# Kernel optimization log

Measured on AMD Instinct MI355X. Metric: run time of the kernel, lower is better.

## Reference

```python
import jax, jax.numpy as jnp
import numpy as np

B, L, HID = 128, 256, 768
HID2 = 2 * HID
CDIM, SDIM, NPROJ = 192, 128, 128
FDIM = CDIM + SDIM + 1
BIG = 1e9  # finite pad so sorted invalid tokens go last without inf/nan issues


def setup_inputs() -> dict:
    key = jax.random.key(0)
    ks = jax.random.split(key, 12)
    H = jax.random.normal(ks[0], (B, L, HID), dtype=jnp.float32)
    tt = jax.random.randint(ks[1], (B, L), 0, 2, dtype=jnp.int32)
    m = jnp.ones((B, L), dtype=jnp.int32)
    s = 1.0 / np.sqrt(HID2)
    Wc = jax.random.uniform(ks[2], (CDIM, HID2), minval=-s, maxval=s, dtype=jnp.float32)
    bc = jax.random.uniform(ks[3], (CDIM,), minval=-s, maxval=s, dtype=jnp.float32)
    Ws = jax.random.uniform(ks[4], (SDIM, HID2), minval=-s, maxval=s, dtype=jnp.float32)
    bs = jax.random.uniform(ks[5], (SDIM,), minval=-s, maxval=s, dtype=jnp.float32)
    gate = jnp.array([0.5], dtype=jnp.float32)
    ln_g = jnp.ones((FDIM,), dtype=jnp.float32)
    ln_b = jnp.zeros((FDIM,), dtype=jnp.float32)
    sc = 1.0 / np.sqrt(FDIM)
    Wcls = jax.random.uniform(ks[6], (2, FDIM), minval=-sc, maxval=sc, dtype=jnp.float32)
    bcls = jax.random.uniform(ks[7], (2,), minval=-sc, maxval=sc, dtype=jnp.float32)
    d = jax.random.normal(ks[8], (NPROJ, HID), dtype=jnp.float32)
    proj_dirs = d / jnp.linalg.norm(d, axis=1, keepdims=True)
    return {"H": H, "tt": tt, "m": m, "Wc": Wc, "bc": bc, "Ws": Ws, "bs": bs,
            "gate": gate, "ln_g": ln_g, "ln_b": ln_b, "Wcls": Wcls, "bcls": bcls,
            "proj_dirs": proj_dirs}


def _forward(H, tt, m, Wc, bc, Ws, bs, gate, ln_g, ln_b, Wcls, bcls, proj_dirs):
    mask0 = (tt == 0) & (m == 1)  # [B,L]
    mask1 = (tt == 1) & (m == 1)
    f0 = mask0.astype(H.dtype)
    f1 = mask1.astype(H.dtype)
    cls = H[:, 0]  # [B,HID]
    mean0 = jnp.einsum('blh,bl->bh', H, f0) / jnp.clip(f0.sum(1, keepdims=True), 1.0)
    mean1 = jnp.einsum('blh,bl->bh', H, f1) / jnp.clip(f1.sum(1, keepdims=True), 1.0)
    rep = jnp.concatenate([cls, mean0 - mean1], axis=1)  # [B,2*HID]
    C = rep @ Wc.T + bc
    S = rep @ Ws.T + bs
    g = jax.nn.sigmoid(gate)  # [1]
    fused = jnp.concatenate([C * (1.0 - g), S * g], axis=1)

    # max-sliced W1 between token-type-0 and token-type-1 token sets, batched.
    P = jnp.einsum('blh,ph->blp', H, proj_dirs)  # [B,L,NPROJ]
    x0 = jnp.sort(jnp.where(mask0[..., None], P, BIG), axis=1)  # valid tokens first
    x1 = jnp.sort(jnp.where(mask1[..., None], P, BIG), axis=1)
    n0 = mask0.sum(1)
    n1 = mask1.sum(1)
    mcnt = jnp.minimum(n0, n1)  # [B]
    rmask = (jnp.arange(L)[None, :] < mcnt[:, None])[..., None]  # [B,L,1]
    diff = jnp.where(rmask, x0, 0.0) - jnp.where(rmask, x1, 0.0)
    mean_abs = jnp.abs(diff).sum(1) / jnp.maximum(mcnt, 1)[:, None].astype(P.dtype)  # [B,NPROJ]
    d_ot = mean_abs.max(axis=1, keepdims=True)  # [B,1]

    feat = jnp.concatenate([fused, d_ot], axis=1)  # [B,FDIM]
    mu = feat.mean(-1, keepdims=True)
    var = feat.var(-1, keepdims=True)
    normed = (feat - mu) * jax.lax.rsqrt(var + 1e-5) * ln_g + ln_b
    return normed @ Wcls.T + bcls  # [B,2]


def reference(H, tt, m, Wc, bc, Ws, bs, gate, ln_g, ln_b, Wcls, bcls, proj_dirs):
    return _forward(H, tt, m, Wc, bc, Ws, bs, gate, ln_g, ln_b, Wcls, bcls, proj_dirs)
```

## Files before the change

kernel.cpp:

```cpp
#include <hip/hip_runtime.h>
#include <cmath>

#define B_   128
#define L_   256
#define HID_ 768
#define HID2_ 1536
#define CDIM_ 192
#define SDIM_ 128
#define NPROJ_ 128
#define FDIM_ 321
#define KSL_ 384
#define PTSTRIDE ((size_t)B_ * NPROJ_ * L_)

typedef __attribute__((ext_vector_type(8))) short bf16x8;
typedef __attribute__((ext_vector_type(4))) float f32x4;

__device__ inline unsigned short bf_hi_trunc(float x) {
    return (unsigned short)(__float_as_uint(x) >> 16);
}
__device__ inline float bf2f(unsigned short s) {
    return __uint_as_float(((unsigned int)s) << 16);
}
__device__ inline unsigned short f2bf_rne(float x) {
    unsigned int u = __float_as_uint(x);
    unsigned int r = (u + 0x7fff + ((u >> 16) & 1)) >> 16;
    return (unsigned short)r;
}

__global__ __launch_bounds__(192) void pre_kernel(
    const float* __restrict__ Pd, unsigned short* __restrict__ Pjh,
    unsigned short* __restrict__ Pjl)
{
    int i = blockIdx.x * 192 + threadIdx.x;
    float4 v = ((const float4*)Pd)[i];
    ushort4 h, l;
    h.x = bf_hi_trunc(v.x); l.x = f2bf_rne(v.x - bf2f(h.x));
    h.y = bf_hi_trunc(v.y); l.y = f2bf_rne(v.y - bf2f(h.y));
    h.z = bf_hi_trunc(v.z); l.z = f2bf_rne(v.z - bf2f(h.z));
    h.w = bf_hi_trunc(v.w); l.w = f2bf_rne(v.w - bf2f(h.w));
    ((ushort4*)Pjh)[i] = h;
    ((ushort4*)Pjl)[i] = l;
}

__device__ inline void stats_bfly(float4 x, float4 y, float fa, float fb,
                                  int kbase, int lane, float* __restrict__ sacc)
{
    float px = x.x * fa + y.x * fb;
    float py = x.y * fa + y.y * fb;
    float pz = x.z * fa + y.z * fb;
    float pw = x.w * fa + y.w * fb;
#pragma unroll
    for (int off = 8; off < 64; off <<= 1) {
        px += __shfl_xor(px, off, 64);
        py += __shfl_xor(py, off, 64);
        pz += __shfl_xor(pz, off, 64);
        pw += __shfl_xor(pw, off, 64);
    }
    if (lane < 8) {
        float* d = &sacc[kbase + lane * 4];
        atomicAdd(d + 0, px);
        atomicAdd(d + 1, py);
        atomicAdd(d + 2, pz);
        atomicAdd(d + 3, pw);
    }
}

#define LDSROW 72
__global__ __launch_bounds__(256, 4) void gemm_mfma(
    const float* __restrict__ H, const unsigned short* __restrict__ Pjh,
    const unsigned short* __restrict__ Pjl, const int* __restrict__ tt,
    const int* __restrict__ mm, float* __restrict__ Ptp,
    float* __restrict__ part)
{
    __shared__ unsigned short Hs[2][64 * LDSROW];
    __shared__ float sacc[KSL_];
    __shared__ float sw[64];

    int tid = threadIdx.x;
    int w = tid >> 6;
    int lane = tid & 63;
    int c = lane & 15;
    int q = lane >> 4;

    int ks     = blockIdx.x & 1;
    int lchunk = (blockIdx.x >> 1) & 3;
    int b      = blockIdx.x >> 3;
    int lbase  = lchunk * 64;

    const float* Hbase = H + ((size_t)(b * L_ + lbase)) * HID_ + ks * KSL_;
    int hrow0 = tid >> 3;
    int hc4   = tid & 7;

    const unsigned short* pjh0 = Pjh + (size_t)(w * 32 + c) * HID_ + ks * KSL_ + q * 8;
    const unsigned short* pjh1 = pjh0 + (size_t)16 * HID_;
    const unsigned short* pjl0 = Pjl + (size_t)(w * 32 + c) * HID_ + ks * KSL_ + q * 8;
    const unsigned short* pjl1 = pjl0 + (size_t)16 * HID_;

    f32x4 acc[2][4] = {};

    float4 hA0, hA1, hB0, hB1;
    uint4 fhA0, fhA1, flA0, flA1;
    uint4 fhB0, fhB1, flB0, flB1;
    uint4 chh0, chh1, cll0, cll1;

#define LOADS(S, T) do {                                                      \
    int k0_ = (T) * 32;                                                       \
    h##S##0 = *(const float4*)(Hbase + (size_t)hrow0 * HID_ + k0_ + hc4 * 4); \
    h##S##1 = *(const float4*)(Hbase + (size_t)(hrow0 + 32) * HID_ + k0_ + hc4 * 4); \
    fh##S##0 = *(const uint4*)(pjh0 + k0_);                                   \
    fh##S##1 = *(const uint4*)(pjh1 + k0_);                                   \
    fl##S##0 = *(const uint4*)(pjl0 + k0_);                                   \
    fl##S##1 = *(const uint4*)(pjl1 + k0_);                                   \
} while (0)

#define CONVST(S, BUF, T) do {                                                \
    float4 v0_ = h##S##0, v1_ = h##S##1;                                      \
    ushort4 h0_, l0_, h1_, l1_;                                               \
    h0_.x = bf_hi_trunc(v0_.x); l0_.x = f2bf_rne(v0_.x - bf2f(h0_.x));        \
    h0_.y = bf_hi_trunc(v0_.y); l0_.y = f2bf_rne(v0_.y - bf2f(h0_.y));        \
    h0_.z = bf_hi_trunc(v0_.z); l0_.z = f2bf_rne(v0_.z - bf2f(h0_.z));        \
    h0_.w = bf_hi_trunc(v0_.w); l0_.w = f2bf_rne(v0_.w - bf2f(h0_.w));        \
    h1_.x = bf_hi_trunc(v1_.x); l1_.x = f2bf_rne(v1_.x - bf2f(h1_.x));        \
    h1_.y = bf_hi_trunc(v1_.y); l1_.y = f2bf_rne(v1_.y - bf2f(h1_.y));        \
    h1_.z = bf_hi_trunc(v1_.z); l1_.z = f2bf_rne(v1_.z - bf2f(h1_.z));        \
    h1_.w = bf_hi_trunc(v1_.w); l1_.w = f2bf_rne(v1_.w - bf2f(h1_.w));        \
    *(ushort4*)&Hs[BUF][hrow0 * LDSROW + hc4 * 4]             = h0_;          \
    *(ushort4*)&Hs[BUF][hrow0 * LDSROW + 32 + hc4 * 4]        = l0_;          \
    *(ushort4*)&Hs[BUF][(hrow0 + 32) * LDSROW + hc4 * 4]      = h1_;          \
    *(ushort4*)&Hs[BUF][(hrow0 + 32) * LDSROW + 32 + hc4 * 4] = l1_;          \
    stats_bfly(v0_, v1_, fa, fb, (T) * 32, lane, sacc);                       \
} while (0)

#define COPYF(S) do {                                                         \
    chh0 = fh##S##0; chh1 = fh##S##1; cll0 = fl##S##0; cll1 = fl##S##1;       \
} while (0)

#define GEMMSTEP(BUF) do {                                                    \
    bf16x8 bh_[4], bl_[4];                                                    \
    _Pragma("unroll")                                                         \
    for (int lt = 0; lt < 4; ++lt) {                                          \
        int l_ = lt * 16 + c;                                                 \
        bh_[lt] = *(const bf16x8*)&Hs[BUF][l_ * LDSROW + q * 8];              \
        bl_[lt] = *(const bf16x8*)&Hs[BUF][l_ * LDSROW + 32 + q * 8];         \
    }                                                                         \
    bf16x8 ah0_ = *(bf16x8*)&chh0, ah1_ = *(bf16x8*)&chh1;                    \
    bf16x8 al0_ = *(bf16x8*)&cll0, al1_ = *(bf16x8*)&cll1;                    \
    _Pragma("unroll")                                                         \
    for (int lt = 0; lt < 4; ++lt) {                                          \
        acc[0][lt] = __builtin_amdgcn_mfma_f32_16x16x32_bf16(ah0_, bh_[lt], acc[0][lt], 0, 0, 0); \
        acc[0][lt] = __builtin_amdgcn_mfma_f32_16x16x32_bf16(ah0_, bl_[lt], acc[0][lt], 0, 0, 0); \
        acc[0][lt] = __builtin_amdgcn_mfma_f32_16x16x32_bf16(al0_, bh_[lt], acc[0][lt], 0, 0, 0); \
        acc[1][lt] = __builtin_amdgcn_mfma_f32_16x16x32_bf16(ah1_, bh_[lt], acc[1][lt], 0, 0, 0); \
        acc[1][lt] = __builtin_amdgcn_mfma_f32_16x16x32_bf16(ah1_, bl_[lt], acc[1][lt], 0, 0, 0); \
        acc[1][lt] = __builtin_amdgcn_mfma_f32_16x16x32_bf16(al1_, bh_[lt], acc[1][lt], 0, 0, 0); \
    }                                                                         \
} while (0)

    LOADS(A, 0);
    LOADS(B, 1);

    int t_ = tt[b * L_ + tid];
    int m_ = mm[b * L_ + tid];
    int n0 = __syncthreads_count(t_ == 0 && m_ == 1);
    int n1 = __syncthreads_count(t_ == 1 && m_ == 1);
    float r0 = 1.f / fmaxf((float)n0, 1.f);
    float r1 = 1.f / fmaxf((float)n1, 1.f);
    if (tid < 64) {
        int tl = tt[b * L_ + lbase + tid];
        int ml = mm[b * L_ + lbase + tid];
        sw[tid] = ((tl == 0 && ml == 1) ? r0 : 0.f)
                - ((tl == 1 && ml == 1) ? r1 : 0.f);
    }
    for (int i = tid; i < KSL_; i += 256) sacc[i] = 0.f;
    __syncthreads();
    float fa = sw[hrow0], fb = sw[hrow0 + 32];

    CONVST(A, 0, 0);
    COPYF(A);
    __syncthreads();

    for (int p = 0; p < 6; ++p) {
        int t0 = 2 * p;
        if (t0 + 2 < 12) LOADS(A, t0 + 2);
        GEMMSTEP(0);
        CONVST(B, 1, t0 + 1);
        COPYF(B);
        __syncthreads();

        int t1 = t0 + 1;
        if (t1 + 2 < 12) LOADS(B, t1 + 2);
        GEMMSTEP(1);
        if (t1 + 1 < 12) {
            CONVST(A, 0, t1 + 1);
            COPYF(A);
        }
        __syncthreads();
    }

    float* Pts = Ptp + (size_t)ks * PTSTRIDE;
#pragma unroll
    for (int pt = 0; pt < 2; ++pt)
#pragma unroll
    for (int lt = 0; lt < 4; ++lt)
#pragma unroll
    for (int r = 0; r < 4; ++r) {
        int p2 = w * 32 + pt * 16 + q * 4 + r;
        int l = lbase + lt * 16 + c;
        Pts[((size_t)(b * NPROJ_ + p2)) * L_ + l] = acc[pt][lt][r];
    }

    {
        float* pdst = part + (size_t)(b * 4 + lchunk) * HID_ + ks * KSL_;
        for (int i = tid; i < KSL_; i += 256)
            pdst[i] = sacc[i];
    }
#undef LOADS
#undef CONVST
#undef COPYF
#undef GEMMSTEP
}

__global__ __launch_bounds__(256) void headot_kernel(
    const float* __restrict__ H, const int* __restrict__ tt,
    const int* __restrict__ mm, const float* __restrict__ part,
    const float* __restrict__ Wc, const float* __restrict__ bc,
    const float* __restrict__ Ws, const float* __restrict__ bs,
    const float* __restrict__ gate, const float* __restrict__ Ptp,
    float* __restrict__ fused, float* __restrict__ dist)
{
    if (blockIdx.x < B_ * 8) {
        __shared__ float srep[HID2_];
        int b = blockIdx.x >> 3;
        int ochunk = (blockIdx.x & 7) * 40;
        int tid = threadIdx.x;

        const float* pp = part + (size_t)b * 4 * HID_;
        for (int h = tid; h < HID_; h += 256) {
            float a = pp[h] + pp[HID_ + h] + pp[2 * HID_ + h] + pp[3 * HID_ + h];
            srep[h]        = H[(size_t)b * L_ * HID_ + h];
            srep[HID_ + h] = a;
        }
        __syncthreads();

        int w = tid >> 6;
        int lane = tid & 63;
        float g = 1.0f / (1.0f + expf(-gate[0]));

#pragma unroll
        for (int r = 0; r < 10; ++r) {
            int o = ochunk + r * 4 + w;
            bool isC = (o < CDIM_);
            const float4* wr = (const float4*)(isC ? (Wc + (size_t)o * HID2_)
                                                   : (Ws + (size_t)(o - CDIM_) * HID2_));
            float acc = 0.f;
#pragma unroll
            for (int u = 0; u < 6; ++u) {
                int k4 = lane + u * 64;
                float4 a = *(const float4*)&srep[k4 * 4];
                float4 ww = wr[k4];
                acc += a.x * ww.x + a.y * ww.y + a.z * ww.z + a.w * ww.w;
            }
            for (int off = 32; off; off >>= 1) acc += __shfl_xor(acc, off, 64);
            if (lane == 0) {
                float bias = isC ? bc[o] : bs[o - CDIM_];
                float scale = isC ? (1.0f - g) : g;
                fused[(size_t)b * (CDIM_ + SDIM_) + o] = (acc + bias) * scale;
            }
        }
        return;
    }

    int bid = blockIdx.x - B_ * 8;
    int w = bid * 4 + (threadIdx.x >> 6);
    int lane = threadIdx.x & 63;
    int b = w >> 7;
    int p = w & (NPROJ_ - 1);

    float4 pv0 = *(const float4*)(Ptp + ((size_t)(b * NPROJ_ + p)) * L_ + lane * 4);
    float4 pv1 = *(const float4*)(Ptp + PTSTRIDE + ((size_t)(b * NPROJ_ + p)) * L_ + lane * 4);
    float4 pv = make_float4(pv0.x + pv1.x, pv0.y + pv1.y, pv0.z + pv1.z, pv0.w + pv1.w);
    int4 t4 = *(const int4*)(tt + (size_t)b * L_ + lane * 4);
    int4 m4 = *(const int4*)(mm + (size_t)b * L_ + lane * 4);

    float pvals[4] = {pv.x, pv.y, pv.z, pv.w};
    int tv[4] = {t4.x, t4.y, t4.z, t4.w};
    int mv[4] = {m4.x, m4.y, m4.z, m4.w};

    unsigned key[4];
#pragma unroll
    for (int r = 0; r < 4; ++r) {
        unsigned u = __float_as_uint(pvals[r]);
        unsigned s = (u & 0x80000000u) ? ~u : (u | 0x80000000u);
        unsigned label = (mv[r] == 1) ? (unsigned)tv[r] : 2u;
        key[r] = (s & ~3u) | label;
    }

    {
        unsigned mn0 = min(key[0], key[1]), mx0 = max(key[0], key[1]);
        key[0] = mn0; key[1] = mx0;
        unsigned mn1 = min(key[2], key[3]), mx1 = max(key[2], key[3]);
        key[2] = mx1; key[3] = mn1;
    }
#pragma unroll
    for (int k = 4; k <= 256; k <<= 1) {
        bool up = (lane & (k >> 2)) == 0;
#pragma unroll
        for (int j = k >> 1; j >= 4; j >>= 1) {
            int lj = j >> 2;
#pragma unroll
            for (int r = 0; r < 4; ++r) {
                unsigned o = (unsigned)__shfl_xor((int)key[r], lj, 64);
                bool lower = (lane & lj) == 0;
                unsigned mn = min(key[r], o), mx = max(key[r], o);
                key[r] = (lower == up) ? mn : mx;
            }
        }
        {
            unsigned mn0 = min(key[0], key[2]), mx0 = max(key[0], key[2]);
            key[0] = up ? mn0 : mx0; key[2] = up ? mx0 : mn0;
            unsigned mn1 = min(key[1], key[3]), mx1 = max(key[1], key[3]);
            key[1] = up ? mn1 : mx1; key[3] = up ? mx1 : mn1;
        }
        {
            unsigned mn0 = min(key[0], key[1]), mx0 = max(key[0], key[1]);
            key[0] = up ? mn0 : mx0; key[1] = up ? mx0 : mn0;
            unsigned mn1 = min(key[2], key[3]), mx1 = max(key[2], key[3]);
            key[2] = up ? mn1 : mx1; key[3] = up ? mx1 : mn1;
        }
    }

    int lab[4];
    float tval[4];
    unsigned sincl[4];
    unsigned run = 0;
#pragma unroll
    for (int r = 0; r < 4; ++r) {
        lab[r] = (int)(key[r] & 3u);
        unsigned s = key[r] & ~3u;
        unsigned u = (s & 0x80000000u) ? (s ^ 0x80000000u) : ~s;
        tval[r] = __uint_as_float(u);
        unsigned unit = ((lab[r] == 0) ? 0x10000u : 0u) | ((lab[r] == 1) ? 1u : 0u);
        run += unit;
        sincl[r] = run;
    }
    unsigned inc = run;
#pragma unroll
    for (int d = 1; d < 64; d <<= 1) {
        unsigned tt2 = (unsigned)__shfl_up((int)inc, d, 64);
        if (lane >= d) inc += tt2;
    }
    unsigned ex = inc - run;
    unsigned total = (unsigned)__shfl((int)inc, 63, 64);
    int n0 = (int)(total >> 16), n1 = (int)(total & 0xffffu);
    int m = (n0 < n1) ? n0 : n1;

    float ssum = 0.f;
#pragma unroll
    for (int r = 0; r < 4; ++r) {
        unsigned C = ex + sincl[r];
        int c0 = (int)(C >> 16), c1 = (int)(C & 0xffffu);
        int s0 = (lab[r] == 0), s1 = (lab[r] == 1);
        int wi = abs(min(c0, m) - min(c1, m));
        int wp = abs(min(c0 - s0, m) - min(c1 - s1, m));
        ssum += tval[r] * (float)(wp - wi);
    }
    for (int off = 32; off; off >>= 1) ssum += __shfl_xor(ssum, off, 64);
    if (lane == 0) dist[b * NPROJ_ + p] = ssum / (float)((m > 1) ? m : 1);
}

__global__ __launch_bounds__(64) void final_kernel(
    const float* __restrict__ fused, const float* __restrict__ dist,
    const float* __restrict__ ln_g, const float* __restrict__ ln_b,
    const float* __restrict__ Wcls, const float* __restrict__ bcls,
    float* __restrict__ out)
{
    int b = blockIdx.x;
    int lane = threadIdx.x;

    float mx = fmaxf(dist[b * NPROJ_ + lane], dist[b * NPROJ_ + 64 + lane]);
    for (int off = 32; off; off >>= 1) mx = fmaxf(mx, __shfl_xor(mx, off, 64));

    float fv[6];
    float sum = 0.f, sq = 0.f;
#pragma unroll
    for (int u = 0; u < 6; ++u) {
        int j = lane + u * 64;
        float x = 0.f;
        if (j < CDIM_ + SDIM_) x = fused[(size_t)b * (CDIM_ + SDIM_) + j];
        else if (j == CDIM_ + SDIM_) x = mx;
        fv[u] = x;
        if (j < FDIM_) { sum += x; sq += x * x; }
    }
    for (int off = 32; off; off >>= 1) {
        sum += __shfl_xor(sum, off, 64);
        sq  += __shfl_xor(sq,  off, 64);
    }
    float mu = sum / (float)FDIM_;
    float var = sq / (float)FDIM_ - mu * mu;
    float inv = rsqrtf(var + 1e-5f);

    float d0 = 0.f, d1 = 0.f;
#pragma unroll
    for (int u = 0; u < 6; ++u) {
        int j = lane + u * 64;
        if (j < FDIM_) {
            float nx = (fv[u] - mu) * inv * ln_g[j] + ln_b[j];
            d0 += nx * Wcls[j];
            d1 += nx * Wcls[FDIM_ + j];
        }
    }
    for (int off = 32; off; off >>= 1) {
        d0 += __shfl_xor(d0, off, 64);
        d1 += __shfl_xor(d1, off, 64);
    }
    if (lane == 0) {
        out[b * 2 + 0] = d0 + bcls[0];
        out[b * 2 + 1] = d1 + bcls[1];
    }
}

extern "C" void kernel_launch(void* const* d_in, const int* in_sizes, int n_in,
                              void* d_out, int out_size, void* d_ws, size_t ws_size,
                              hipStream_t stream)
{
    const float* H    = (const float*)d_in[0];
    const int*   tt   = (const int*)d_in[1];
    const int*   mm   = (const int*)d_in[2];
    const float* Wc   = (const float*)d_in[3];
    const float* bc   = (const float*)d_in[4];
    const float* Ws   = (const float*)d_in[5];
    const float* bs   = (const float*)d_in[6];
    const float* gate = (const float*)d_in[7];
    const float* ln_g = (const float*)d_in[8];
    const float* ln_b = (const float*)d_in[9];
    const float* Wcls = (const float*)d_in[10];
    const float* bcls = (const float*)d_in[11];
    const float* Pd   = (const float*)d_in[12];
    float* out = (float*)d_out;

    float* ws = (float*)d_ws;
    float* Ptp   = ws;
    float* part  = Ptp + 2 * PTSTRIDE;
    float* fused = part + (size_t)B_ * 4 * HID_;
    float* dist  = fused + (size_t)B_ * (CDIM_ + SDIM_);
    unsigned short* Pjh = (unsigned short*)(dist + (size_t)B_ * NPROJ_);
    unsigned short* Pjl = Pjh + (size_t)NPROJ_ * HID_;

    pre_kernel<<<128, 192, 0, stream>>>(Pd, Pjh, Pjl);
    gemm_mfma<<<B_ * 8, 256, 0, stream>>>(H, Pjh, Pjl, tt, mm, Ptp, part);
    headot_kernel<<<B_ * 8 + B_ * NPROJ_ / 4, 256, 0, stream>>>(
        H, tt, mm, part, Wc, bc, Ws, bs, gate, Ptp, fused, dist);
    final_kernel<<<B_, 64, 0, stream>>>(fused, dist, ln_g, ln_b, Wcls, bcls, out);
}
```

Baseline: 246.5 us.

## Widen GEMM K-step to 64 with single-stage prefetch and halved barriers

Restructures the split-bf16 MFMA projection GEMM to process 64-wide K tiles per iteration instead of 32, cutting the loop from 12 to 6 steps and halving the number of __syncthreads barriers. The two-deep register prefetch (A/B sets) is replaced by a one-tile-ahead prefetch of double-size tiles, and the LDS row stride grows to hold 64 hi plus 64 lo values. Occupancy hint drops from 4 to 3 blocks per CU to accommodate the larger register and LDS footprint, which may reduce latency hiding.

```diff
diff --git a/kernel.cpp b/kernel.cpp
--- a/kernel.cpp
+++ b/kernel.cpp
@@ -65,14 +65,14 @@
     }
 }
 
-#define LDSROW 72
-__global__ __launch_bounds__(256, 4) void gemm_mfma(
+#define LDSROW64 136
+__global__ __launch_bounds__(256, 3) void gemm_mfma(
     const float* __restrict__ H, const unsigned short* __restrict__ Pjh,
     const unsigned short* __restrict__ Pjl, const int* __restrict__ tt,
     const int* __restrict__ mm, float* __restrict__ Ptp,
     float* __restrict__ part)
 {
-    __shared__ unsigned short Hs[2][64 * LDSROW];
+    __shared__ unsigned short Hs[2][64 * LDSROW64];
     __shared__ float sacc[KSL_];
     __shared__ float sw[64];
 
@@ -97,67 +97,83 @@
     const unsigned short* pjl1 = pjl0 + (size_t)16 * HID_;
 
     f32x4 acc[2][4] = {};
-
-    float4 hA0, hA1, hB0, hB1;
-    uint4 fhA0, fhA1, flA0, flA1;
-    uint4 fhB0, fhB1, flB0, flB1;
-    uint4 chh0, chh1, cll0, cll1;
-
-#define LOADS(S, T) do {                                                      \
-    int k0_ = (T) * 32;                                                       \
-    h##S##0 = *(const float4*)(Hbase + (size_t)hrow0 * HID_ + k0_ + hc4 * 4); \
-    h##S##1 = *(const float4*)(Hbase + (size_t)(hrow0 + 32) * HID_ + k0_ + hc4 * 4); \
-    fh##S##0 = *(const uint4*)(pjh0 + k0_);                                   \
-    fh##S##1 = *(const uint4*)(pjh1 + k0_);                                   \
-    fl##S##0 = *(const uint4*)(pjl0 + k0_);                                   \
-    fl##S##1 = *(const uint4*)(pjl1 + k0_);                                   \
+    float4 h0a, h0b, h1a, h1b;
+    uint4 cah[2][2], cal[2][2];
+    uint4 nah[2][2], nal[2][2];
+
+#define LOADT(T) do {                                                         \
+    int k0_ = (T) * 64;                                                       \
+    h0a = *(const float4*)(Hbase + (size_t)hrow0 * HID_ + k0_ + hc4 * 4);     \
+    h0b = *(const float4*)(Hbase + (size_t)hrow0 * HID_ + k0_ + 32 + hc4 * 4);\
+    h1a = *(const float4*)(Hbase + (size_t)(hrow0 + 32) * HID_ + k0_ + hc4 * 4);      \
+    h1b = *(const float4*)(Hbase + (size_t)(hrow0 + 32) * HID_ + k0_ + 32 + hc4 * 4); \
+    nah[0][0] = *(const uint4*)(pjh0 + k0_);                                  \
+    nah[0][1] = *(const uint4*)(pjh0 + k0_ + 32);                             \
+    nah[1][0] = *(const uint4*)(pjh1 + k0_);                                  \
+    nah[1][1] = *(const uint4*)(pjh1 + k0_ + 32);                             \
+    nal[0][0] = *(const uint4*)(pjl0 + k0_);                                  \
+    nal[0][1] = *(const uint4*)(pjl0 + k0_ + 32);                             \
+    nal[1][0] = *(const uint4*)(pjl1 + k0_);                                  \
+    nal[1][1] = *(const uint4*)(pjl1 + k0_ + 32);                             \
 } while (0)
 
-#define CONVST(S, BUF, T) do {                                                \
-    float4 v0_ = h##S##0, v1_ = h##S##1;                                      \
-    ushort4 h0_, l0_, h1_, l1_;                                               \
-    h0_.x = bf_hi_trunc(v0_.x); l0_.x = f2bf_rne(v0_.x - bf2f(h0_.x));        \
-    h0_.y = bf_hi_trunc(v0_.y); l0_.y = f2bf_rne(v0_.y - bf2f(h0_.y));        \
-    h0_.z = bf_hi_trunc(v0_.z); l0_.z = f2bf_rne(v0_.z - bf2f(h0_.z));        \
-    h0_.w = bf_hi_trunc(v0_.w); l0_.w = f2bf_rne(v0_.w - bf2f(h0_.w));        \
-    h1_.x = bf_hi_trunc(v1_.x); l1_.x = f2bf_rne(v1_.x - bf2f(h1_.x));        \
-    h1_.y = bf_hi_trunc(v1_.y); l1_.y = f2bf_rne(v1_.y - bf2f(h1_.y));        \
-    h1_.z = bf_hi_trunc(v1_.z); l1_.z = f2bf_rne(v1_.z - bf2f(h1_.z));        \
-    h1_.w = bf_hi_trunc(v1_.w); l1_.w = f2bf_rne(v1_.w - bf2f(h1_.w));        \
-    *(ushort4*)&Hs[BUF][hrow0 * LDSROW + hc4 * 4]             = h0_;          \
-    *(ushort4*)&Hs[BUF][hrow0 * LDSROW + 32 + hc4 * 4]        = l0_;          \
-    *(ushort4*)&Hs[BUF][(hrow0 + 32) * LDSROW + hc4 * 4]      = h1_;          \
-    *(ushort4*)&Hs[BUF][(hrow0 + 32) * LDSROW + 32 + hc4 * 4] = l1_;          \
-    stats_bfly(v0_, v1_, fa, fb, (T) * 32, lane, sacc);                       \
+#define CVT1(V, HH, LL) do {                                                  \
+    HH.x = bf_hi_trunc(V.x); LL.x = f2bf_rne(V.x - bf2f(HH.x));               \
+    HH.y = bf_hi_trunc(V.y); LL.y = f2bf_rne(V.y - bf2f(HH.y));               \
+    HH.z = bf_hi_trunc(V.z); LL.z = f2bf_rne(V.z - bf2f(HH.z));               \
+    HH.w = bf_hi_trunc(V.w); LL.w = f2bf_rne(V.w - bf2f(HH.w));               \
 } while (0)
 
-#define COPYF(S) do {                                                         \
-    chh0 = fh##S##0; chh1 = fh##S##1; cll0 = fl##S##0; cll1 = fl##S##1;       \
+#define CONVT(BUF, T) do {                                                    \
+    ushort4 hh_, ll_;                                                         \
+    CVT1(h0a, hh_, ll_);                                                      \
+    *(ushort4*)&Hs[BUF][hrow0 * LDSROW64 + hc4 * 4]      = hh_;               \
+    *(ushort4*)&Hs[BUF][hrow0 * LDSROW64 + 64 + hc4 * 4] = ll_;               \
+    CVT1(h0b, hh_, ll_);                                                      \
+    *(ushort4*)&Hs[BUF][hrow0 * LDSROW64 + 32 + hc4 * 4] = hh_;               \
+    *(ushort4*)&Hs[BUF][hrow0 * LDSROW64 + 96 + hc4 * 4] = ll_;               \
+    CVT1(h1a, hh_, ll_);                                                      \
+    *(ushort4*)&Hs[BUF][(hrow0 + 32) * LDSROW64 + hc4 * 4]      = hh_;        \
+    *(ushort4*)&Hs[BUF][(hrow0 + 32) * LDSROW64 + 64 + hc4 * 4] = ll_;        \
+    CVT1(h1b, hh_, ll_);                                                      \
+    *(ushort4*)&Hs[BUF][(hrow0 + 32) * LDSROW64 + 32 + hc4 * 4] = hh_;        \
+    *(ushort4*)&Hs[BUF][(hrow0 + 32) * LDSROW64 + 96 + hc4 * 4] = ll_;        \
+    stats_bfly(h0a, h1a, fa, fb, (T) * 64,      lane, sacc);                  \
+    stats_bfly(h0b, h1b, fa, fb, (T) * 64 + 32, lane, sacc);                  \
 } while (0)
 
-#define GEMMSTEP(BUF) do {                                                    \
-    bf16x8 bh_[4], bl_[4];                                                    \
+#define COPYNC do {                                                           \
+    cah[0][0] = nah[0][0]; cah[0][1] = nah[0][1];                             \
+    cah[1][0] = nah[1][0]; cah[1][1] = nah[1][1];                             \
+    cal[0][0] = nal[0][0]; cal[0][1] = nal[0][1];                             \
+    cal[1][0] = nal[1][0]; cal[1][1] = nal[1][1];                             \
+} while (0)
+
+#define GEMM64(BUF) do {                                                      \
     _Pragma("unroll")                                                         \
-    for (int lt = 0; lt < 4; ++lt) {                                          \
-        int l_ = lt * 16 + c;                                                 \
-        bh_[lt] = *(const bf16x8*)&Hs[BUF][l_ * LDSROW + q * 8];              \
-        bl_[lt] = *(const bf16x8*)&Hs[BUF][l_ * LDSROW + 32 + q * 8];         \
-    }                                                                         \
-    bf16x8 ah0_ = *(bf16x8*)&chh0, ah1_ = *(bf16x8*)&chh1;                    \
-    bf16x8 al0_ = *(bf16x8*)&cll0, al1_ = *(bf16x8*)&cll1;                    \
-    _Pragma("unroll")                                                         \
-    for (int lt = 0; lt < 4; ++lt) {                                          \
-        acc[0][lt] = __builtin_amdgcn_mfma_f32_16x16x32_bf16(ah0_, bh_[lt], acc[0][lt], 0, 0, 0); \
-        acc[0][lt] = __builtin_amdgcn_mfma_f32_16x16x32_bf16(ah0_, bl_[lt], acc[0][lt], 0, 0, 0); \
-        acc[0][lt] = __builtin_amdgcn_mfma_f32_16x16x32_bf16(al0_, bh_[lt], acc[0][lt], 0, 0, 0); \
-        acc[1][lt] = __builtin_amdgcn_mfma_f32_16x16x32_bf16(ah1_, bh_[lt], acc[1][lt], 0, 0, 0); \
-        acc[1][lt] = __builtin_amdgcn_mfma_f32_16x16x32_bf16(ah1_, bl_[lt], acc[1][lt], 0, 0, 0); \
-        acc[1][lt] = __builtin_amdgcn_mfma_f32_16x16x32_bf16(al1_, bh_[lt], acc[1][lt], 0, 0, 0); \
+    for (int kk = 0; kk < 2; ++kk) {                                          \
+        bf16x8 bh_[4], bl_[4];                                                \
+        _Pragma("unroll")                                                     \
+        for (int lt = 0; lt < 4; ++lt) {                                      \
+            int l_ = lt * 16 + c;                                             \
+            bh_[lt] = *(const bf16x8*)&Hs[BUF][l_ * LDSROW64 + kk * 32 + q * 8];      \
+            bl_[lt] = *(const bf16x8*)&Hs[BUF][l_ * LDSROW64 + 64 + kk * 32 + q * 8]; \
+        }                                                                     \
+        _Pragma("unroll")                                                     \
+        for (int pt = 0; pt < 2; ++pt) {                                      \
+            bf16x8 ah_ = *(bf16x8*)&cah[pt][kk];                              \
+            bf16x8 al_ = *(bf16x8*)&cal[pt][kk];                              \
+            _Pragma("unroll")                                                 \
+            for (int lt = 0; lt < 4; ++lt) {                                  \
+                acc[pt][lt] = __builtin_amdgcn_mfma_f32_16x16x32_bf16(ah_, bh_[lt], acc[pt][lt], 0, 0, 0); \
+                acc[pt][lt] = __builtin_amdgcn_mfma_f32_16x16x32_bf16(ah_, bl_[lt], acc[pt][lt], 0, 0, 0); \
+                acc[pt][lt] = __builtin_amdgcn_mfma_f32_16x16x32_bf16(al_, bh_[lt], acc[pt][lt], 0, 0, 0); \
+            }                                                                 \
+        }                                                                     \
     }                                                                         \
 } while (0)
 
-    LOADS(A, 0);
-    LOADS(B, 1);
+    LOADT(0);
 
     int t_ = tt[b * L_ + tid];
     int m_ = mm[b * L_ + tid];
@@ -175,24 +191,19 @@
     __syncthreads();
     float fa = sw[hrow0], fb = sw[hrow0 + 32];
 
-    CONVST(A, 0, 0);
-    COPYF(A);
+    COPYNC;
+    CONVT(0, 0);
     __syncthreads();
 
-    for (int p = 0; p < 6; ++p) {
-        int t0 = 2 * p;
-        if (t0 + 2 < 12) LOADS(A, t0 + 2);
-        GEMMSTEP(0);
-        CONVST(B, 1, t0 + 1);
-        COPYF(B);
-        __syncthreads();
-
-        int t1 = t0 + 1;
-        if (t1 + 2 < 12) LOADS(B, t1 + 2);
-        GEMMSTEP(1);
-        if (t1 + 1 < 12) {
-            CONVST(A, 0, t1 + 1);
-            COPYF(A);
+    for (int it = 0; it < 6; ++it) {
+        int cur = it & 1;
+        int nxt = cur ^ 1;
+
+        if (it + 1 < 6) LOADT(it + 1);
+        GEMM64(cur);
+        if (it + 1 < 6) {
+            CONVT(nxt, it + 1);
+            COPYNC;
         }
         __syncthreads();
     }
@@ -214,10 +225,11 @@
         for (int i = tid; i < KSL_; i += 256)
             pdst[i] = sacc[i];
     }
-#undef LOADS
-#undef CONVST
-#undef COPYF
-#undef GEMMSTEP
+#undef LOADT
+#undef CVT1
+#undef CONVT
+#undef COPYNC
+#undef GEMM64
 }
 
 __global__ __launch_bounds__(256) void headot_kernel(
```

Result: faster. 219.7 us (-10.9%).
